# Kernel optimization log

Measured on AMD Instinct MI355X. Metric: run time of the kernel, lower is better.

Reference implementation:

```python
import jax, jax.numpy as jnp
import numpy as np

B, T, NCH, NBIN, NBAND = 2, 400, 8, 512, 40
NPV = NCH * NCH


def setup_inputs() -> dict:
    key = jax.random.key(0)
    ks = jax.random.split(key, 7)
    bins_real = jax.random.normal(ks[0], (B, T, NCH, NBIN), jnp.float32)
    bins_imag = jax.random.normal(ks[1], (B, T, NCH, NBIN), jnp.float32)
    band_matrix_real = jax.random.normal(ks[2], (NBIN, NBAND), jnp.float32) * 0.05
    band_matrix_imag = jax.random.normal(ks[3], (NBIN, NBAND), jnp.float32) * 0.05
    cov_to_pv_real = jax.random.normal(ks[4], (NPV, NCH * NCH), jnp.float32) * 0.1
    cov_to_pv_imag = jax.random.normal(ks[5], (NPV, NCH * NCH), jnp.float32) * 0.1
    tau = jax.random.uniform(ks[6], (NBAND,), jnp.float32, 0.8, 0.99)
    return {
        'bins_real': bins_real, 'bins_imag': bins_imag,
        'band_matrix_real': band_matrix_real, 'band_matrix_imag': band_matrix_imag,
        'cov_to_pv_real': cov_to_pv_real, 'cov_to_pv_imag': cov_to_pv_imag,
        'tau': tau,
    }


def _power_vector(bins_real, bins_imag, band_matrix_real, band_matrix_imag,
                  cov_to_pv_real, cov_to_pv_imag, tau):
    x = jax.lax.complex(bins_real, bins_imag)            # (B,T,C,F)
    nch = x.shape[-2]
    EPS = 1e-20
    # per-bin covariance outer product, flattened cov dim: (B,T,F,C*C)
    cov = jnp.einsum('btif,btjf->btfij', x, jnp.conj(x))
    b, t, f = cov.shape[:3]
    cov = cov.reshape(b, t, f, nch * nch)
    diag = jnp.arange(nch) * (nch + 1)                   # diagonal indices in cov dim
    trace = jnp.clip(jnp.sum(cov.real[..., diag], axis=-1, keepdims=True), EPS, None)
    cov = cov / trace                                    # per-bin trace normalisation
    # phase adjustment along the bin axis (n=1 -> lag of 2 bins)
    c = jnp.swapaxes(cov, -1, -2)                        # (B,T,C2,F)
    prod = jnp.conj(c[..., :-2]) * c[..., 2:]
    ang = jnp.arctan2(prod.imag, prod.real)
    ang = jnp.concatenate([ang[..., :1], ang, ang[..., -1:]], axis=-1)  # edge pad
    adj = jnp.abs(c) * jax.lax.complex(jnp.cos(ang), jnp.sin(ang))
    adj = adj.at[..., diag, :].set(c[..., diag, :])      # keep original diagonals
    # band projection: contract bins against (F,K) band matrix
    bm = jax.lax.complex(band_matrix_real, band_matrix_imag)
    band_cov = jnp.einsum('btcf,fk->btkc', adj, bm)      # (B,T,K,C2)
    dsum = jnp.clip(band_cov.real[..., diag].sum(-1, keepdims=True), EPS, None)
    band_cov = band_cov / dsum
    # first-order IIR smoothing over frames, per-band pole tau
    a = tau[:, None].astype(band_cov.real.dtype)         # (K,1)
    def step(carry, xt):
        y = a * carry + (1.0 - a) * xt
        return y, y
    y0 = jnp.zeros_like(band_cov[:, 0])                  # (B,K,C2)
    _, ys = jax.lax.scan(step, y0, jnp.moveaxis(band_cov, 1, 0))
    band_cov = jnp.moveaxis(ys, 0, 1)                    # (B,T,K,C2)
    # cov -> power vector projection, real part
    c2p = jax.lax.complex(cov_to_pv_real, cov_to_pv_imag)  # (P,C2)
    pv = jnp.einsum('pc,btkc->btkp', c2p, band_cov).real   # (B,T,K,P)
    return pv


def reference(bins_real, bins_imag, band_matrix_real, band_matrix_imag,
              cov_to_pv_real, cov_to_pv_imag, tau):
    return _power_vector(bins_real, bins_imag, band_matrix_real, band_matrix_imag,
                         cov_to_pv_real, cov_to_pv_imag, tau)
```

## Files before the change

### kernel.cpp

```cpp
#include <hip/hip_runtime.h>
#include <hip/hip_fp16.h>

#define B_    2
#define T_    400
#define NCH_  8
#define NBIN_ 512
#define NBAND_ 40
#define NPV_  64

using half8   = __attribute__((ext_vector_type(8))) _Float16;
using float4v = __attribute__((ext_vector_type(4))) float;

static __device__ inline unsigned pkhf(float x, float y) {
  __half2 h = __float22half2_rn(make_float2(x, y));
  return __builtin_bit_cast(unsigned, h);
}
static __device__ inline unsigned rot16(unsigned u) {
  return (u >> 16) | (u << 16);
}
static __device__ inline unsigned cmulc(unsigned viu, unsigned vju) {
  __half2 Vi = __builtin_bit_cast(__half2, viu);
  __half2 Vj = __builtin_bit_cast(__half2, vju);
  __half2 P1 = __hmul2(Vi, __low2half2(Vj));
  __half2 Qi = __lowhigh2highlow(Vi);
  unsigned tn = __builtin_bit_cast(unsigned, __high2half2(Vj)) ^ 0x80000000u;
  __half2 a  = __hfma2(Qi, __builtin_bit_cast(__half2, tn), P1);
  return __builtin_bit_cast(unsigned, a);
}
static __device__ inline void gld_lds16(const uint4* g, uint4* l) {
  auto* lds_ptr = reinterpret_cast<__attribute__((address_space(3))) uint4*>(
      reinterpret_cast<uintptr_t>(l));
  auto* g_ptr = reinterpret_cast<const __attribute__((address_space(1))) uint4*>(
      reinterpret_cast<uintptr_t>(g));
  __builtin_amdgcn_global_load_lds(g_ptr, lds_ptr, 16, 0, 0);
}

__global__ __launch_bounds__(256) void pv_prep(
    const float* __restrict__ bmr, const float* __restrict__ bmi,
    const float* __restrict__ c2pr, const float* __restrict__ c2pi,
    float* __restrict__ ws)
{
  const int tid = threadIdx.x;
  const int blk = blockIdx.x;
  if (blk == 0) {
    __shared__ float sds[256];
    int k = tid & 63, part = tid >> 6;
    float s = 0.f;
    if (k < NBAND_) {
      const float* col = bmr + k;
      #pragma unroll 16
      for (int f = part * 128; f < part * 128 + 128; f++) s += col[f * 40];
    }
    sds[tid] = s;
    __syncthreads();
    if (tid < NBAND_) {
      float t = sds[tid] + sds[tid + 64] + sds[tid + 128] + sds[tid + 192];
      ws[tid] = 1.0f / fmaxf(t, 1e-20f);
    }
  } else if (blk <= 24) {
    int F = (blk - 1) * 256 + tid;
    int l = F & 63;
    int fid = F >> 6;
    int s5 = fid / 3;
    int n = fid - s5 * 3;
    int k = n * 16 + (l & 15);
    int quad = l >> 4;
    unsigned dw[4];
    #pragma unroll
    for (int t2 = 0; t2 < 4; t2++) {
      float v0 = 0.f, v1 = 0.f;
      if (k < NBAND_) {
        int f = s5 * 16 + quad * 4 + t2;
        v0 = bmr[f * 40 + k]; v1 = bmi[f * 40 + k];
      }
      dw[t2] = pkhf(v0, v1);
    }
    ((uint4*)((char*)ws + 1024))[F] = make_uint4(dw[0], dw[1], dw[2], dw[3]);
  } else {
    int F2 = (blk - 25) * 256 + tid;
    int lane = F2 & 63, E = F2 >> 6;
    int nt = E >> 2, ks = E & 3;
    int n = lane & 15, quad = lane >> 4;
    int p = nt * 16 + n;
    unsigned dw[4];
    #pragma unroll
    for (int t2 = 0; t2 < 4; t2++) {
      int c = ks * 16 + quad * 4 + t2;
      dw[t2] = pkhf(c2pr[p * 64 + c], -c2pi[p * 64 + c]);
    }
    ((uint4*)((char*)ws + 197632))[E * 64 + lane] = make_uint4(dw[0], dw[1], dw[2], dw[3]);
  }
}

__global__ __launch_bounds__(256, 2) void pv_main(
    const float* __restrict__ br, const float* __restrict__ bi,
    const float* __restrict__ ws, float* __restrict__ out)
{
  __shared__ __align__(16) unsigned smem[14336];
  unsigned* vshA[2] = { smem, smem + 4096 };
  uint4*    bst = (uint4*)(smem + 8192);

  const int bt0 = blockIdx.x * 2;
  const int tid = threadIdx.x;

  const int mt   = tid >> 6;
  const int lane = tid & 63;
  const int m16  = lane & 15;
  const int quad = lane >> 4;
  const int p    = mt * 16 + m16;
  const int ich  = p >> 3, jch = p & 7;
  const uint4* BF0 = (const uint4*)((const char*)ws + 1024);

  {
    const uint4* g = BF0 + tid;
    uint4* l = bst + tid;
    gld_lds16(g, l);
    gld_lds16(g + 256, l + 256);
    gld_lds16(g + 512, l + 512);
  }

  #pragma unroll
  for (int h = 0; h < 2; h++) {
    const float* pr  = br + (size_t)(bt0 + h) * (NCH_ * NBIN_);
    const float* pim = bi + (size_t)(bt0 + h) * (NCH_ * NBIN_);
    unsigned* vsh = vshA[h];
    #pragma unroll
    for (int fs = 0; fs < 2; fs++) {
      const int f = fs * 256 + tid;
      const int fm = (f == 0) ? 0 : ((f == 511) ? 509 : f - 1);
      const int fp = (f == 0) ? 2 : ((f == 511) ? 511 : f + 1);
      float tr = 0.f;
      float t1[8], t2[8];
      #pragma unroll
      for (int c = 0; c < 8; c++) {
        const float* cr = pr + c * 512;
        const float* ci = pim + c * 512;
        float xr = cr[f],   xi = ci[f];
        float xrm = cr[fm], xim = ci[fm];
        float xrp = cr[fp], xip = ci[fp];
        tr = fmaf(xr, xr, tr); tr = fmaf(xi, xi, tr);
        float Gr = fmaf(xrm, xrp,  xim * xip);
        float Gi = fmaf(xrm, xip, -(xim * xrp));
        float am = fmaxf(fmaxf(fabsf(Gr), fabsf(Gi)), 1e-30f);
        float rc = __builtin_amdgcn_rcpf(am);
        float q1 = Gr * rc, q2 = Gi * rc;
        float n2 = fmaf(q1, q1, q2 * q2);
        float rn = __builtin_amdgcn_rsqf(n2);
        bool ok = n2 > 0.f;
        float ur = ok ? q1 * rn : 1.f;
        float ui = ok ? q2 * rn : 0.f;
        float mg = __builtin_amdgcn_sqrtf(fmaf(xr, xr, xi * xi));
        t1[c] = mg * ur; t2[c] = mg * ui;
      }
      float scv = __builtin_amdgcn_rsqf(fmaxf(tr, 1e-20f));
      const int fc = f >> 2, fl = f & 3;
      #pragma unroll
      for (int c = 0; c < 8; c++)
        vsh[c * 512 + ((fc ^ c) << 2) + fl] = pkhf(t1[c] * scv, t2[c] * scv);
    }
  }
  __syncthreads();

  float4v acc[12];
  #pragma unroll
  for (int g = 0; g < 12; g++) acc[g] = (float4v){0.f, 0.f, 0.f, 0.f};

  for (int st = 0; st < 8; st++) {
    if (st < 7) {
      const uint4* g = BF0 + (st + 1) * 768 + tid;
      uint4* l = bst + ((st + 1) & 1) * 768 + tid;
      gld_lds16(g, l);
      gld_lds16(g + 256, l + 256);
      gld_lds16(g + 512, l + 512);
    }
    const uint4* bb = bst + (st & 1) * 768;
    #pragma unroll
    for (int q = 0; q < 4; q++) {
      const int s = st * 4 + q;
      const int sc = s * 4 + quad;
      uint4 cb0 = bb[(q * 3 + 0) * 64 + lane];
      uint4 cb1 = bb[(q * 3 + 1) * 64 + lane];
      uint4 cb2 = bb[(q * 3 + 2) * 64 + lane];
      half8 b0 = __builtin_bit_cast(half8, cb0);
      half8 b1 = __builtin_bit_cast(half8, cb1);
      half8 b2 = __builtin_bit_cast(half8, cb2);
      #pragma unroll
      for (int h = 0; h < 2; h++) {
        const uint4* vb = (const uint4*)vshA[h];
        uint4 av = vb[ich * 128 + (sc ^ ich)];
        uint4 bv = vb[jch * 128 + (sc ^ jch)];
        unsigned a0 = cmulc(av.x, bv.x);
        unsigned a1 = cmulc(av.y, bv.y);
        unsigned a2 = cmulc(av.z, bv.z);
        unsigned a3 = cmulc(av.w, bv.w);
        uint4 au1 = make_uint4(a0 ^ 0x80000000u, a1 ^ 0x80000000u,
                               a2 ^ 0x80000000u, a3 ^ 0x80000000u);
        uint4 au2 = make_uint4(rot16(a0), rot16(a1),
                               rot16(a2), rot16(a3));
        half8 af1 = __builtin_bit_cast(half8, au1);
        half8 af2 = __builtin_bit_cast(half8, au2);
        acc[h*6+0] = __builtin_amdgcn_mfma_f32_16x16x32_f16(af1, b0, acc[h*6+0], 0, 0, 0);
        acc[h*6+3] = __builtin_amdgcn_mfma_f32_16x16x32_f16(af2, b0, acc[h*6+3], 0, 0, 0);
        acc[h*6+1] = __builtin_amdgcn_mfma_f32_16x16x32_f16(af1, b1, acc[h*6+1], 0, 0, 0);
        acc[h*6+4] = __builtin_amdgcn_mfma_f32_16x16x32_f16(af2, b1, acc[h*6+4], 0, 0, 0);
        acc[h*6+2] = __builtin_amdgcn_mfma_f32_16x16x32_f16(af1, b2, acc[h*6+2], 0, 0, 0);
        acc[h*6+5] = __builtin_amdgcn_mfma_f32_16x16x32_f16(af2, b2, acc[h*6+5], 0, 0, 0);
      }
    }
    __syncthreads();
  }

  const uint4* EF = ((const uint4*)((const char*)ws + 197632)) + (mt * 4) * 64 + lane;
  uint4 eb[4];
  #pragma unroll
  for (int ks = 0; ks < 4; ks++) eb[ks] = EF[ks * 64];

  #pragma unroll
  for (int h = 0; h < 2; h++) {
    unsigned* bcsh = vshA[h];
    #pragma unroll
    for (int n = 0; n < 3; n++) {
      uint4 w4 = make_uint4(pkhf(acc[h*6+n][0], acc[h*6+n+3][0]),
                            pkhf(acc[h*6+n][1], acc[h*6+n+3][1]),
                            pkhf(acc[h*6+n][2], acc[h*6+n+3][2]),
                            pkhf(acc[h*6+n][3], acc[h*6+n+3][3]));
      *(uint4*)(bcsh + (n * 16 + m16) * 68 + mt * 16 + quad * 4) = w4;
    }
  }
  __syncthreads();

  const float4* wsd = (const float4*)ws;
  #pragma unroll
  for (int h = 0; h < 2; h++) {
    const unsigned* bcsh = vshA[h];
    float4v eacc[3];
    #pragma unroll
    for (int kt = 0; kt < 3; kt++) eacc[kt] = (float4v){0.f, 0.f, 0.f, 0.f};
    #pragma unroll
    for (int ks = 0; ks < 4; ks++) {
      half8 bfr = __builtin_bit_cast(half8, eb[ks]);
      #pragma unroll
      for (int kt = 0; kt < 3; kt++) {
        uint4 a4 = *(const uint4*)(bcsh + (kt * 16 + m16) * 68 + ks * 16 + quad * 4);
        half8 afr = __builtin_bit_cast(half8, a4);
        eacc[kt] = __builtin_amdgcn_mfma_f32_16x16x32_f16(afr, bfr, eacc[kt], 0, 0, 0);
      }
    }
    float* op = out + (size_t)(bt0 + h) * (NBAND_ * NPV_);
    #pragma unroll
    for (int kt = 0; kt < 3; kt++) {
      float4 dv = wsd[kt * 4 + quad];
      float dva[4] = {dv.x, dv.y, dv.z, dv.w};
      #pragma unroll
      for (int r = 0; r < 4; r++) {
        int k = kt * 16 + quad * 4 + r;
        if (k < NBAND_)
          op[k * 64 + mt * 16 + m16] = eacc[kt][r] * dva[r];
      }
    }
  }
}

__global__ __launch_bounds__(640) void pv_iir4(float* __restrict__ z,
                                               const float* __restrict__ tau)
{
  __shared__ float gsh[40][16];
  const int pg = blockIdx.x & 3;
  const int bk = blockIdx.x >> 2;
  const int k = bk % NBAND_;
  const int b = bk / NBAND_;
  const float a  = tau[k];
  const float om = 1.0f - a;
  const int c  = threadIdx.x >> 4;
  const int pl = threadIdx.x & 15;
  const int p  = pg * 16 + pl;
  const size_t stride = (size_t)NBAND_ * 64;
  size_t idx0 = (size_t)b * (T_ * NBAND_ * 64) + (size_t)(c * 10) * stride + k * 64 + p;

  float y[10];
  float accv = 0.f;
  #pragma unroll
  for (int i = 0; i < 10; i++) {
    float v = z[idx0 + (size_t)i * stride];
    accv = fmaf(a, accv, om * v);
    y[i] = accv;
  }
  gsh[c][pl] = accv;
  __syncthreads();
  float a2 = a * a, a4 = a2 * a2, a8 = a4 * a4;
  float A = a8 * a2;
  float H = 0.f;
  #pragma unroll
  for (int d = 0; d < 39; d++) {
    float g = gsh[d][pl];
    H = (d < c) ? fmaf(A, H, g) : H;
  }
  float wp = a;
  #pragma unroll
  for (int i = 0; i < 10; i++) {
    z[idx0 + (size_t)i * stride] = fmaf(wp, H, y[i]);
    wp *= a;
  }
}

extern "C" void kernel_launch(void* const* d_in, const int* in_sizes, int n_in,
                              void* d_out, int out_size, void* d_ws, size_t ws_size,
                              hipStream_t stream)
{
  const float* br   = (const float*)d_in[0];
  const float* bi   = (const float*)d_in[1];
  const float* bmr  = (const float*)d_in[2];
  const float* bmi  = (const float*)d_in[3];
  const float* c2pr = (const float*)d_in[4];
  const float* c2pi = (const float*)d_in[5];
  const float* tau  = (const float*)d_in[6];
  float* out = (float*)d_out;
  float* ws  = (float*)d_ws;

  hipLaunchKernelGGL(pv_prep, dim3(29), dim3(256), 0, stream,
                     bmr, bmi, c2pr, c2pi, ws);
  hipLaunchKernelGGL(pv_main, dim3(B_ * T_ / 2), dim3(256), 0, stream,
                     br, bi, ws, out);
  hipLaunchKernelGGL(pv_iir4, dim3(B_ * NBAND_ * 4), dim3(640), 0, stream,
                     out, tau);
}
```

Before: 114.7 us.

## Fuse IIR smoothing into main kernel via software grid barrier

```diff
diff --git a/kernel.cpp b/kernel.cpp
--- a/kernel.cpp
+++ b/kernel.cpp
@@ -43,6 +43,7 @@
   const int tid = threadIdx.x;
   const int blk = blockIdx.x;
   if (blk == 0) {
+    if (tid < 2) ((unsigned*)ws)[64 + tid] = 0u;
     __shared__ float sds[256];
     int k = tid & 63, part = tid >> 6;
     float s = 0.f;
@@ -92,9 +93,10 @@
   }
 }
 
-__global__ __launch_bounds__(256, 2) void pv_main(
+__global__ __launch_bounds__(256, 2) void pv_fused(
     const float* __restrict__ br, const float* __restrict__ bi,
-    const float* __restrict__ ws, float* __restrict__ out)
+    const float* __restrict__ ws, float* __restrict__ out,
+    const float* __restrict__ tau)
 {
   __shared__ __align__(16) unsigned smem[14336];
   unsigned* vshA[2] = { smem, smem + 4096 };
@@ -259,46 +261,63 @@
       }
     }
   }
-}
-
-__global__ __launch_bounds__(640) void pv_iir4(float* __restrict__ z,
-                                               const float* __restrict__ tau)
-{
-  __shared__ float gsh[40][16];
-  const int pg = blockIdx.x & 3;
-  const int bk = blockIdx.x >> 2;
-  const int k = bk % NBAND_;
-  const int b = bk / NBAND_;
+
+  {
+    unsigned* bar = (unsigned*)ws + 64;
+    __syncthreads();
+    if (tid == 0) {
+      __threadfence();
+      unsigned prev = __hip_atomic_fetch_add(&bar[0], 1u, __ATOMIC_ACQ_REL,
+                                             __HIP_MEMORY_SCOPE_AGENT);
+      if (prev == (unsigned)(gridDim.x - 1)) {
+        __hip_atomic_store(&bar[1], 1u, __ATOMIC_RELEASE,
+                           __HIP_MEMORY_SCOPE_AGENT);
+      } else {
+        while (__hip_atomic_load(&bar[1], __ATOMIC_ACQUIRE,
+                                 __HIP_MEMORY_SCOPE_AGENT) == 0u)
+          __builtin_amdgcn_s_sleep(8);
+      }
+    }
+    __syncthreads();
+  }
+
+  const int blk = blockIdx.x;
+  if (blk >= B_ * NBAND_ * 4) return;
+  const int pg = blk & 3;
+  const int bk = blk >> 2;
+  const int k  = bk % NBAND_;
+  const int b  = bk / NBAND_;
   const float a  = tau[k];
   const float om = 1.0f - a;
-  const int c  = threadIdx.x >> 4;
-  const int pl = threadIdx.x & 15;
-  const int p  = pg * 16 + pl;
+  const int c  = tid >> 4;
+  const int pl = tid & 15;
   const size_t stride = (size_t)NBAND_ * 64;
-  size_t idx0 = (size_t)b * (T_ * NBAND_ * 64) + (size_t)(c * 10) * stride + k * 64 + p;
-
-  float y[10];
+  size_t idx0 = (size_t)b * (T_ * NBAND_ * 64) + (size_t)(c * 25) * stride
+              + (size_t)k * 64 + (size_t)(pg * 16 + pl);
+
+  float* gsh = (float*)smem;
+  float y[25];
   float accv = 0.f;
   #pragma unroll
-  for (int i = 0; i < 10; i++) {
-    float v = z[idx0 + (size_t)i * stride];
+  for (int i = 0; i < 25; i++) {
+    float v = out[idx0 + (size_t)i * stride];
     accv = fmaf(a, accv, om * v);
     y[i] = accv;
   }
-  gsh[c][pl] = accv;
+  gsh[c * 16 + pl] = accv;
   __syncthreads();
-  float a2 = a * a, a4 = a2 * a2, a8 = a4 * a4;
-  float A = a8 * a2;
+  float a2 = a * a, a4 = a2 * a2, a8 = a4 * a4, a16 = a8 * a8;
+  float A = a16 * a8 * a;
   float H = 0.f;
   #pragma unroll
-  for (int d = 0; d < 39; d++) {
-    float g = gsh[d][pl];
+  for (int d = 0; d < 15; d++) {
+    float g = gsh[d * 16 + pl];
     H = (d < c) ? fmaf(A, H, g) : H;
   }
   float wp = a;
   #pragma unroll
-  for (int i = 0; i < 10; i++) {
-    z[idx0 + (size_t)i * stride] = fmaf(wp, H, y[i]);
+  for (int i = 0; i < 25; i++) {
+    out[idx0 + (size_t)i * stride] = fmaf(wp, H, y[i]);
     wp *= a;
   }
 }
@@ -319,8 +338,6 @@
 
   hipLaunchKernelGGL(pv_prep, dim3(29), dim3(256), 0, stream,
                      bmr, bmi, c2pr, c2pi, ws);
-  hipLaunchKernelGGL(pv_main, dim3(B_ * T_ / 2), dim3(256), 0, stream,
-                     br, bi, ws, out);
-  hipLaunchKernelGGL(pv_iir4, dim3(B_ * NBAND_ * 4), dim3(640), 0, stream,
-                     out, tau);
-}
+  hipLaunchKernelGGL(pv_fused, dim3(B_ * T_ / 2), dim3(256), 0, stream,
+                     br, bi, ws, out, tau);
+}
```

New measurement: 166.7 us. +45.3%, slower.

## Load band-matrix fragments from global into registers instead of LDS staging

Applied to the files above, without the earlier changes.

```diff
diff --git a/kernel.cpp b/kernel.cpp
--- a/kernel.cpp
+++ b/kernel.cpp
@@ -26,13 +26,6 @@
   unsigned tn = __builtin_bit_cast(unsigned, __high2half2(Vj)) ^ 0x80000000u;
   __half2 a  = __hfma2(Qi, __builtin_bit_cast(__half2, tn), P1);
   return __builtin_bit_cast(unsigned, a);
-}
-static __device__ inline void gld_lds16(const uint4* g, uint4* l) {
-  auto* lds_ptr = reinterpret_cast<__attribute__((address_space(3))) uint4*>(
-      reinterpret_cast<uintptr_t>(l));
-  auto* g_ptr = reinterpret_cast<const __attribute__((address_space(1))) uint4*>(
-      reinterpret_cast<uintptr_t>(g));
-  __builtin_amdgcn_global_load_lds(g_ptr, lds_ptr, 16, 0, 0);
 }
 
 __global__ __launch_bounds__(256) void pv_prep(
@@ -92,13 +85,12 @@
   }
 }
 
-__global__ __launch_bounds__(256, 2) void pv_main(
+__global__ __launch_bounds__(256, 4) void pv_main(
     const float* __restrict__ br, const float* __restrict__ bi,
     const float* __restrict__ ws, float* __restrict__ out)
 {
-  __shared__ __align__(16) unsigned smem[14336];
+  __shared__ __align__(16) unsigned smem[8192];
   unsigned* vshA[2] = { smem, smem + 4096 };
-  uint4*    bst = (uint4*)(smem + 8192);
 
   const int bt0 = blockIdx.x * 2;
   const int tid = threadIdx.x;
@@ -110,14 +102,6 @@
   const int p    = mt * 16 + m16;
   const int ich  = p >> 3, jch = p & 7;
   const uint4* BF0 = (const uint4*)((const char*)ws + 1024);
-
-  {
-    const uint4* g = BF0 + tid;
-    uint4* l = bst + tid;
-    gld_lds16(g, l);
-    gld_lds16(g + 256, l + 256);
-    gld_lds16(g + 512, l + 512);
-  }
 
   #pragma unroll
   for (int h = 0; h < 2; h++) {
@@ -165,50 +149,43 @@
   #pragma unroll
   for (int g = 0; g < 12; g++) acc[g] = (float4v){0.f, 0.f, 0.f, 0.f};
 
-  for (int st = 0; st < 8; st++) {
-    if (st < 7) {
-      const uint4* g = BF0 + (st + 1) * 768 + tid;
-      uint4* l = bst + ((st + 1) & 1) * 768 + tid;
-      gld_lds16(g, l);
-      gld_lds16(g + 256, l + 256);
-      gld_lds16(g + 512, l + 512);
-    }
-    const uint4* bb = bst + (st & 1) * 768;
-    #pragma unroll
-    for (int q = 0; q < 4; q++) {
-      const int s = st * 4 + q;
-      const int sc = s * 4 + quad;
-      uint4 cb0 = bb[(q * 3 + 0) * 64 + lane];
-      uint4 cb1 = bb[(q * 3 + 1) * 64 + lane];
-      uint4 cb2 = bb[(q * 3 + 2) * 64 + lane];
-      half8 b0 = __builtin_bit_cast(half8, cb0);
-      half8 b1 = __builtin_bit_cast(half8, cb1);
-      half8 b2 = __builtin_bit_cast(half8, cb2);
-      #pragma unroll
-      for (int h = 0; h < 2; h++) {
-        const uint4* vb = (const uint4*)vshA[h];
-        uint4 av = vb[ich * 128 + (sc ^ ich)];
-        uint4 bv = vb[jch * 128 + (sc ^ jch)];
-        unsigned a0 = cmulc(av.x, bv.x);
-        unsigned a1 = cmulc(av.y, bv.y);
-        unsigned a2 = cmulc(av.z, bv.z);
-        unsigned a3 = cmulc(av.w, bv.w);
-        uint4 au1 = make_uint4(a0 ^ 0x80000000u, a1 ^ 0x80000000u,
-                               a2 ^ 0x80000000u, a3 ^ 0x80000000u);
-        uint4 au2 = make_uint4(rot16(a0), rot16(a1),
-                               rot16(a2), rot16(a3));
-        half8 af1 = __builtin_bit_cast(half8, au1);
-        half8 af2 = __builtin_bit_cast(half8, au2);
-        acc[h*6+0] = __builtin_amdgcn_mfma_f32_16x16x32_f16(af1, b0, acc[h*6+0], 0, 0, 0);
-        acc[h*6+3] = __builtin_amdgcn_mfma_f32_16x16x32_f16(af2, b0, acc[h*6+3], 0, 0, 0);
-        acc[h*6+1] = __builtin_amdgcn_mfma_f32_16x16x32_f16(af1, b1, acc[h*6+1], 0, 0, 0);
-        acc[h*6+4] = __builtin_amdgcn_mfma_f32_16x16x32_f16(af2, b1, acc[h*6+4], 0, 0, 0);
-        acc[h*6+2] = __builtin_amdgcn_mfma_f32_16x16x32_f16(af1, b2, acc[h*6+2], 0, 0, 0);
-        acc[h*6+5] = __builtin_amdgcn_mfma_f32_16x16x32_f16(af2, b2, acc[h*6+5], 0, 0, 0);
-      }
-    }
-    __syncthreads();
-  }
+  const uint4* Bg = BF0 + lane;
+  uint4 nb0 = Bg[0], nb1 = Bg[64], nb2 = Bg[128];
+  #pragma unroll 4
+  for (int s = 0; s < 32; s++) {
+    uint4 cb0 = nb0, cb1 = nb1, cb2 = nb2;
+    {
+      const uint4* nx = Bg + (size_t)(((s + 1) & 31) * 192);
+      nb0 = nx[0]; nb1 = nx[64]; nb2 = nx[128];
+    }
+    const int sc = s * 4 + quad;
+    half8 b0 = __builtin_bit_cast(half8, cb0);
+    half8 b1 = __builtin_bit_cast(half8, cb1);
+    half8 b2 = __builtin_bit_cast(half8, cb2);
+    #pragma unroll
+    for (int h = 0; h < 2; h++) {
+      const uint4* vb = (const uint4*)vshA[h];
+      uint4 av = vb[ich * 128 + (sc ^ ich)];
+      uint4 bv = vb[jch * 128 + (sc ^ jch)];
+      unsigned a0 = cmulc(av.x, bv.x);
+      unsigned a1 = cmulc(av.y, bv.y);
+      unsigned a2 = cmulc(av.z, bv.z);
+      unsigned a3 = cmulc(av.w, bv.w);
+      uint4 au1 = make_uint4(a0 ^ 0x80000000u, a1 ^ 0x80000000u,
+                             a2 ^ 0x80000000u, a3 ^ 0x80000000u);
+      uint4 au2 = make_uint4(rot16(a0), rot16(a1),
+                             rot16(a2), rot16(a3));
+      half8 af1 = __builtin_bit_cast(half8, au1);
+      half8 af2 = __builtin_bit_cast(half8, au2);
+      acc[h*6+0] = __builtin_amdgcn_mfma_f32_16x16x32_f16(af1, b0, acc[h*6+0], 0, 0, 0);
+      acc[h*6+3] = __builtin_amdgcn_mfma_f32_16x16x32_f16(af2, b0, acc[h*6+3], 0, 0, 0);
+      acc[h*6+1] = __builtin_amdgcn_mfma_f32_16x16x32_f16(af1, b1, acc[h*6+1], 0, 0, 0);
+      acc[h*6+4] = __builtin_amdgcn_mfma_f32_16x16x32_f16(af2, b1, acc[h*6+4], 0, 0, 0);
+      acc[h*6+2] = __builtin_amdgcn_mfma_f32_16x16x32_f16(af1, b2, acc[h*6+2], 0, 0, 0);
+      acc[h*6+5] = __builtin_amdgcn_mfma_f32_16x16x32_f16(af2, b2, acc[h*6+5], 0, 0, 0);
+    }
+  }
+  __syncthreads();
 
   const uint4* EF = ((const uint4*)((const char*)ws + 197632)) + (mt * 4) * 64 + lane;
   uint4 eb[4];
```

After: 117.2 us. +2.2%, slower.
